# Optimization experiments

Measured on AMD Instinct MI355X. Metric: run time of the kernel, lower is better.

The kernel has to match this reference:

```python
import jax, jax.numpy as jnp
import numpy as np

NUM_ROI = 400
N_GRAPHS = 128
N_NODES = NUM_ROI * N_GRAPHS            # 51200
N_EDGES = N_NODES * 40                  # 2048000
EMB = [128, 128]
BN_EPS = 1e-5


def mish(x):
    return x * jnp.tanh(jax.nn.softplus(x))


def gcn_conv(x, row, col, ew, W, b, n_nodes):
    """PyG GCNConv: h = XW; add self-loops (w=1); sym-normalize; scatter-add; + bias."""
    h = x @ W                                            # [N, out]
    loops = jnp.arange(n_nodes, dtype=row.dtype)
    row_ = jnp.concatenate([row, loops])
    col_ = jnp.concatenate([col, loops])
    ew_ = jnp.concatenate([ew, jnp.ones((n_nodes,), ew.dtype)])
    deg = jax.ops.segment_sum(ew_, col_, num_segments=n_nodes)
    dinv = jnp.where(deg > 0, jax.lax.rsqrt(deg), 0.0)
    norm = dinv[row_] * ew_ * dinv[col_]                 # [E+N]
    msg = norm[:, None] * h[row_]                        # gather + scale
    out = jax.ops.segment_sum(msg, col_, num_segments=n_nodes)
    return out + b


def setup_inputs() -> dict:
    key = jax.random.key(0)
    ks = jax.random.split(key, 16)
    inp = {
        "x": jax.random.normal(ks[0], (N_NODES, NUM_ROI), jnp.float32),
        "edge_index": jax.random.randint(ks[1], (2, N_EDGES), 0, N_NODES, jnp.int64)
        if jax.config.jax_enable_x64 else jax.random.randint(ks[1], (2, N_EDGES), 0, N_NODES, jnp.int32),
        "edge_attr": jax.random.uniform(ks[2], (N_EDGES,), jnp.float32),
        "batch": jnp.repeat(jnp.arange(N_GRAPHS), NUM_ROI),
        "conv1_w": jax.random.normal(ks[3], (NUM_ROI, EMB[0]), jnp.float32) * 0.05,
        "conv1_b": jax.random.normal(ks[4], (EMB[0],), jnp.float32) * 0.05,
        "conv2_w": jax.random.normal(ks[5], (EMB[0], EMB[1]), jnp.float32) * 0.05,
        "conv2_b": jax.random.normal(ks[6], (EMB[1],), jnp.float32) * 0.05,
        "ro_w": jax.random.normal(ks[7], (EMB[1], 8), jnp.float32) * 0.05,
        "ro_b": jax.random.normal(ks[8], (8,), jnp.float32) * 0.05,
        "fc1_w": jax.random.normal(ks[9], (8 * NUM_ROI, NUM_ROI), jnp.float32) * 0.02,
        "fc1_b": jax.random.normal(ks[10], (NUM_ROI,), jnp.float32) * 0.02,
        "bn_gamma": jnp.ones((NUM_ROI,), jnp.float32),
        "bn_beta": jnp.zeros((NUM_ROI,), jnp.float32),
        "fc2_w": jax.random.normal(ks[11], (NUM_ROI, 2), jnp.float32) * 0.05,
        "fc2_b": jax.random.normal(ks[12], (2,), jnp.float32) * 0.05,
    }
    return inp


def reference(x, edge_index, edge_attr, batch,
              conv1_w, conv1_b, conv2_w, conv2_b,
              ro_w, ro_b, fc1_w, fc1_b, bn_gamma, bn_beta, fc2_w, fc2_b):
    n = x.shape[0]
    row, col = edge_index[0], edge_index[1]
    h = mish(gcn_conv(x, row, col, edge_attr, conv1_w, conv1_b, n))
    h = mish(gcn_conv(h, row, col, edge_attr, conv2_w, conv2_b, n))
    out = mish(h @ ro_w + ro_b)                          # [N, 8]
    feats = out.reshape(-1, NUM_ROI * 8)                 # [B, 3200]
    z = feats @ fc1_w + fc1_b                            # [B, 400]
    # BatchNorm1d (training mode: batch statistics, biased variance)
    mu = jnp.mean(z, axis=0)
    var = jnp.mean((z - mu) ** 2, axis=0)
    zn = (z - mu) * jax.lax.rsqrt(var + BN_EPS) * bn_gamma + bn_beta
    logits = mish(zn) @ fc2_w + fc2_b                    # [B, 2]
    return logits
```

## Files before the change

### kernel.cpp

```cpp
#include <hip/hip_runtime.h>
#include <hip/hip_fp16.h>
#include <math.h>

#define NN 51200
#define NE 2048000
#define F 128
#define NB 1000
#define EPB 2048
#define NBKT 200

typedef _Float16 half8 __attribute__((ext_vector_type(8)));
typedef float floatx4 __attribute__((ext_vector_type(4)));

__device__ __forceinline__ float mish_f(float x) {
  if (x > 20.0f) return x;
  float e = __expf(x);
  float w = 1.0f + e;
  w = w * w;
  return x * (w - 1.0f) / (w + 1.0f);
}

__global__ __launch_bounds__(256) void k_chist(const int* __restrict__ ei, unsigned* __restrict__ G) {
  __shared__ unsigned hist[NBKT];
  int blk = blockIdx.x, t = threadIdx.x;
  for (int i = t; i < NBKT; i += 256) hist[i] = 0u;
  __syncthreads();
  int base = blk * EPB;
  for (int it = 0; it < EPB; it += 256) {
    int dst = ei[NE + base + it + t];
    atomicAdd(&hist[dst >> 8], 1u);
  }
  __syncthreads();
  for (int i = t; i < NBKT; i += 256) G[(size_t)i * NB + blk] = hist[i];
}

__global__ __launch_bounds__(64) void k_bscan(unsigned* __restrict__ G, unsigned* __restrict__ btot) {
  int b = blockIdx.x, l = threadIdx.x;
  unsigned base = (unsigned)l * 16;
  unsigned loc[16];
  unsigned s = 0;
#pragma unroll
  for (int i = 0; i < 16; ++i) {
    unsigned idx = base + i;
    unsigned x = (idx < NB) ? G[(size_t)b * NB + idx] : 0u;
    loc[i] = s;
    s += x;
  }
  unsigned run = s;
#pragma unroll
  for (int off = 1; off < 64; off <<= 1) {
    unsigned y = __shfl_up(run, off);
    if (l >= off) run += y;
  }
  unsigned excl = run - s;
#pragma unroll
  for (int i = 0; i < 16; ++i) {
    unsigned idx = base + i;
    if (idx < NB) G[(size_t)b * NB + idx] = excl + loc[i];
  }
  if (l == 63) btot[b] = run;
}

__global__ __launch_bounds__(256) void k_bbase(const unsigned* __restrict__ btot, unsigned* __restrict__ bbase) {
  int t = threadIdx.x, lane = t & 63, wid = t >> 6;
  unsigned v = (t < NBKT) ? btot[t] : 0u;
  unsigned x = v;
#pragma unroll
  for (int off = 1; off < 64; off <<= 1) {
    unsigned y = __shfl_up(x, off);
    if (lane >= off) x += y;
  }
  __shared__ unsigned ws4[4];
  if (lane == 63) ws4[wid] = x;
  __syncthreads();
  unsigned woff = 0;
  for (int k = 0; k < wid; ++k) woff += ws4[k];
  if (t < NBKT) bbase[t] = woff + x - v;
  if (t == 255) bbase[NBKT] = woff + x;
}

__global__ __launch_bounds__(256) void k_cscat(const int* __restrict__ ei, const float* __restrict__ ew,
                                               const unsigned* __restrict__ G,
                                               const unsigned* __restrict__ bbase,
                                               uint2* __restrict__ E) {
  __shared__ unsigned cur[NBKT];
  int blk = blockIdx.x, t = threadIdx.x;
  for (int i = t; i < NBKT; i += 256) cur[i] = bbase[i] + G[(size_t)i * NB + blk];
  __syncthreads();
  int base = blk * EPB;
  for (int it = 0; it < EPB; it += 256) {
    int e = base + it + t;
    int dst = ei[NE + e];
    int src = ei[e];
    float w = ew[e];
    unsigned pos = atomicAdd(&cur[dst >> 8], 1u);
    E[pos] = make_uint2((unsigned)src | ((unsigned)(dst & 255) << 16), __float_as_uint(w));
  }
}

__global__ __launch_bounds__(256) void k_fcnt(const uint2* __restrict__ E, const unsigned* __restrict__ bbase,
                                              int* __restrict__ cnt, float* __restrict__ dinv) {
  __shared__ unsigned lc[256];
  __shared__ float ld[256];
  int b = blockIdx.x, t = threadIdx.x;
  lc[t] = 0u;
  ld[t] = 0.f;
  __syncthreads();
  unsigned e0 = bbase[b], e1 = bbase[b + 1];
  for (unsigned e = e0 + t; e < e1; e += 256) {
    uint2 v = E[e];
    unsigned node = (v.x >> 16) & 255u;
    atomicAdd(&lc[node], 1u);
    atomicAdd(&ld[node], __uint_as_float(v.y));
  }
  __syncthreads();
  cnt[b * 256 + t] = (int)lc[t];
  dinv[b * 256 + t] = rsqrtf(ld[t] + 1.0f);
}

__global__ __launch_bounds__(256) void k_scan1(const int* __restrict__ cnt, int* __restrict__ bsum) {
  int i = blockIdx.x * 256 + threadIdx.x;
  int s = cnt[i];
#pragma unroll
  for (int off = 1; off < 64; off <<= 1) s += __shfl_xor(s, off);
  __shared__ int wsum[4];
  if ((threadIdx.x & 63) == 0) wsum[threadIdx.x >> 6] = s;
  __syncthreads();
  if (threadIdx.x == 0) bsum[blockIdx.x] = wsum[0] + wsum[1] + wsum[2] + wsum[3];
}

__global__ __launch_bounds__(256) void k_scan2(const int* __restrict__ bsum, int* __restrict__ boff,
                                               int* __restrict__ rowptr) {
  int t = threadIdx.x;
  int lane = t & 63, wid = t >> 6;
  int v = (t < 200) ? bsum[t] : 0;
  int x = v;
#pragma unroll
  for (int off = 1; off < 64; off <<= 1) {
    int y = __shfl_up(x, off);
    if (lane >= off) x += y;
  }
  __shared__ int ws4[4];
  if (lane == 63) ws4[wid] = x;
  __syncthreads();
  int woff = 0;
  for (int k = 0; k < wid; ++k) woff += ws4[k];
  if (t < 200) boff[t] = woff + x - v;
  if (t == 255) rowptr[NN] = woff + x;
}

__global__ __launch_bounds__(256) void k_scan3(const int* __restrict__ cnt, const int* __restrict__ boff,
                                               int* __restrict__ rowptr) {
  int i = blockIdx.x * 256 + threadIdx.x;
  int t = threadIdx.x;
  int lane = t & 63, wid = t >> 6;
  int v = cnt[i];
  int x = v;
#pragma unroll
  for (int off = 1; off < 64; off <<= 1) {
    int y = __shfl_up(x, off);
    if (lane >= off) x += y;
  }
  __shared__ int ws4[4];
  if (lane == 63) ws4[wid] = x;
  __syncthreads();
  int woff = boff[blockIdx.x];
  for (int k = 0; k < wid; ++k) woff += ws4[k];
  rowptr[i] = woff + x - v;
}

__global__ __launch_bounds__(256) void k_fscat(const uint2* __restrict__ E, const unsigned* __restrict__ bbase,
                                               const int* __restrict__ rowptr, const float* __restrict__ dinv,
                                               int2* __restrict__ csr) {
  __shared__ int cur[256];
  int b = blockIdx.x, t = threadIdx.x;
  cur[t] = rowptr[b * 256 + t];
  __syncthreads();
  unsigned e0 = bbase[b], e1 = bbase[b + 1];
  for (unsigned e = e0 + t; e < e1; e += 256) {
    uint2 v = E[e];
    unsigned node = (v.x >> 16) & 255u;
    int src = (int)(v.x & 0xFFFFu);
    float w = dinv[src] * __uint_as_float(v.y);
    int p = atomicAdd(&cur[node], 1);
    csr[p] = make_int2(src, __float_as_int(w));
  }
}

__global__ void k_prep_w(const float* __restrict__ W, _Float16* __restrict__ Wt, int K) {
  int idx = blockIdx.x * blockDim.x + threadIdx.x;
  if (idx < K * 128) {
    int k = idx >> 7, n = idx & 127;
    Wt[n * K + k] = (_Float16)W[idx];
  }
}

template <bool A_IS_F32>
__global__ __launch_bounds__(256) void k_gemm16(const void* __restrict__ Av,
                                                const _Float16* __restrict__ Wt,
                                                __half* __restrict__ C, int K) {
  __shared__ _Float16 As[128][40];
  __shared__ _Float16 Bs[128][40];
  int t = threadIdx.x;
  int bm = blockIdx.x * 128;
  int w = t >> 6, l = t & 63, rr = l & 15, q = l >> 4;
  int si = t >> 1, sj = (t & 1) * 16;

  floatx4 acc[2][8];
#pragma unroll
  for (int a = 0; a < 2; ++a)
#pragma unroll
    for (int b = 0; b < 8; ++b) acc[a][b] = (floatx4){0.f, 0.f, 0.f, 0.f};

  for (int k0 = 0; k0 < K; k0 += 32) {
    if (A_IS_F32) {
      const float* A = (const float*)Av;
      half8 h0, h1;
      if (k0 + sj < K) {
        const float* ap = A + (size_t)(bm + si) * K + k0 + sj;
        float4 v0 = *(const float4*)(ap + 0);
        float4 v1 = *(const float4*)(ap + 4);
        float4 v2 = *(const float4*)(ap + 8);
        float4 v3 = *(const float4*)(ap + 12);
        h0 = (half8){(_Float16)v0.x, (_Float16)v0.y, (_Float16)v0.z, (_Float16)v0.w,
                     (_Float16)v1.x, (_Float16)v1.y, (_Float16)v1.z, (_Float16)v1.w};
        h1 = (half8){(_Float16)v2.x, (_Float16)v2.y, (_Float16)v2.z, (_Float16)v2.w,
                     (_Float16)v3.x, (_Float16)v3.y, (_Float16)v3.z, (_Float16)v3.w};
      } else {
        h0 = (half8){0, 0, 0, 0, 0, 0, 0, 0};
        h1 = h0;
      }
      *(half8*)&As[si][sj] = h0;
      *(half8*)&As[si][sj + 8] = h1;
    } else {
      const __half* A = (const __half*)Av;
      uint4 u0, u1;
      if (k0 + sj < K) {
        const __half* ap = A + (size_t)(bm + si) * K + k0 + sj;
        u0 = *(const uint4*)ap;
        u1 = *(const uint4*)(ap + 8);
      } else {
        u0 = make_uint4(0, 0, 0, 0);
        u1 = u0;
      }
      *(uint4*)&As[si][sj] = u0;
      *(uint4*)&As[si][sj + 8] = u1;
    }
    {
      uint4 u0, u1;
      if (k0 + sj < K) {
        const _Float16* wp = Wt + (size_t)si * K + k0 + sj;
        u0 = *(const uint4*)wp;
        u1 = *(const uint4*)(wp + 8);
      } else {
        u0 = make_uint4(0, 0, 0, 0);
        u1 = u0;
      }
      *(uint4*)&Bs[si][sj] = u0;
      *(uint4*)&Bs[si][sj + 8] = u1;
    }
    __syncthreads();

    half8 a0 = *(const half8*)&As[w * 32 + rr][q * 8];
    half8 a1 = *(const half8*)&As[w * 32 + 16 + rr][q * 8];
#pragma unroll
    for (int nt = 0; nt < 8; ++nt) {
      half8 b = *(const half8*)&Bs[nt * 16 + rr][q * 8];
      acc[0][nt] = __builtin_amdgcn_mfma_f32_16x16x32_f16(a0, b, acc[0][nt], 0, 0, 0);
      acc[1][nt] = __builtin_amdgcn_mfma_f32_16x16x32_f16(a1, b, acc[1][nt], 0, 0, 0);
    }
    __syncthreads();
  }
#pragma unroll
  for (int mt = 0; mt < 2; ++mt)
#pragma unroll
    for (int nt = 0; nt < 8; ++nt)
#pragma unroll
      for (int r4 = 0; r4 < 4; ++r4) {
        int row = bm + w * 32 + mt * 16 + q * 4 + r4;
        C[(size_t)row * 128 + nt * 16 + rr] = __float2half(acc[mt][nt][r4]);
      }
}

__global__ __launch_bounds__(256) void k_agg(const __half2* __restrict__ h, const int* __restrict__ rowptr,
                                             const int2* __restrict__ csr, const float* __restrict__ dinv,
                                             const float* __restrict__ bias, __half2* __restrict__ out) {
  unsigned lane = threadIdx.x & 63u;
  int n = blockIdx.x * 4 + (threadIdx.x >> 6);
  float di = dinv[n];
  float2 self = __half22float2(h[((unsigned)n << 6) + lane]);
  float sx = 0.f, sy = 0.f;
  int p = __builtin_amdgcn_readfirstlane(rowptr[n]);
  int p1 = __builtin_amdgcn_readfirstlane(rowptr[n + 1]);
  for (; p + 16 <= p1; p += 16) {
    int2 c[16];
#pragma unroll
    for (int u = 0; u < 16; ++u) c[u] = csr[p + u];
    float2 f[16];
#pragma unroll
    for (int u = 0; u < 16; ++u) f[u] = __half22float2(h[((unsigned)c[u].x << 6) + lane]);
#pragma unroll
    for (int u = 0; u < 16; ++u) {
      float w = __int_as_float(c[u].y);
      sx += w * f[u].x;
      sy += w * f[u].y;
    }
  }
  for (; p + 4 <= p1; p += 4) {
    int2 c[4];
#pragma unroll
    for (int u = 0; u < 4; ++u) c[u] = csr[p + u];
    float2 f[4];
#pragma unroll
    for (int u = 0; u < 4; ++u) f[u] = __half22float2(h[((unsigned)c[u].x << 6) + lane]);
#pragma unroll
    for (int u = 0; u < 4; ++u) {
      float w = __int_as_float(c[u].y);
      sx += w * f[u].x;
      sy += w * f[u].y;
    }
  }
  for (; p < p1; ++p) {
    int2 c0 = csr[p];
    float2 f0 = __half22float2(h[((unsigned)c0.x << 6) + lane]);
    float w = __int_as_float(c0.y);
    sx += w * f0.x;
    sy += w * f0.y;
  }
  float ax = di * (di * self.x + sx);
  float ay = di * (di * self.y + sy);
  float2 bb = ((const float2*)bias)[lane];
  out[((unsigned)n << 6) + lane] = __floats2half2_rn(mish_f(ax + bb.x), mish_f(ay + bb.y));
}

__global__ __launch_bounds__(256) void k_ro(const __half2* __restrict__ h, const float* __restrict__ rw,
                                            const float* __restrict__ rb, float* __restrict__ o8) {
  __shared__ float w[128 * 8];
  int t = threadIdx.x;
  for (int i = t; i < 1024; i += 256) w[i] = rw[i];
  __syncthreads();
  int n = blockIdx.x * 32 + (t >> 3);
  int k = t & 7;
  const __half2* hr = h + (size_t)n * 64;
  float acc = rb[k];
#pragma unroll 4
  for (int j = 0; j < 64; ++j) {
    float2 hv = __half22float2(hr[j]);
    acc += hv.x * w[(2 * j) * 8 + k] + hv.y * w[(2 * j + 1) * 8 + k];
  }
  o8[(size_t)n * 8 + k] = mish_f(acc);
}

__global__ void k_fc1_init(const float* __restrict__ b, float* __restrict__ z) {
  int i = blockIdx.x * blockDim.x + threadIdx.x;
  if (i < 128 * 400) z[i] = b[i % 400];
}

__global__ __launch_bounds__(448) void k_fc1(const float* __restrict__ feats, const float* __restrict__ w,
                                             float* __restrict__ z) {
  __shared__ float fs[8][128];
  int t = threadIdx.x;
  int kc = blockIdx.x * 128;
  int g0 = blockIdx.y * 8;
  for (int i = t; i < 1024; i += 448) {
    int g = i >> 7, k = i & 127;
    fs[g][k] = feats[(size_t)(g0 + g) * 3200 + kc + k];
  }
  __syncthreads();
  if (t < 400) {
    float a[8];
#pragma unroll
    for (int g = 0; g < 8; ++g) a[g] = 0.0f;
    for (int k = 0; k < 128; ++k) {
      float wv = w[(size_t)(kc + k) * 400 + t];
#pragma unroll
      for (int g = 0; g < 8; ++g) a[g] += fs[g][k] * wv;
    }
#pragma unroll
    for (int g = 0; g < 8; ++g) atomicAdd(&z[(size_t)(g0 + g) * 400 + t], a[g]);
  }
}

__global__ __launch_bounds__(128) void k_bn(const float* __restrict__ z, const float* __restrict__ gamma,
                                            const float* __restrict__ beta, float* __restrict__ gs,
                                            float* __restrict__ gb) {
  int j = blockIdx.x;
  int b = threadIdx.x;
  float v = z[b * 400 + j];
  float s = v, s2 = v * v;
#pragma unroll
  for (int off = 1; off < 64; off <<= 1) {
    s += __shfl_xor(s, off);
    s2 += __shfl_xor(s2, off);
  }
  __shared__ float ls[2], ls2[2];
  if ((b & 63) == 0) {
    ls[b >> 6] = s;
    ls2[b >> 6] = s2;
  }
  __syncthreads();
  if (b == 0) {
    float mu = (ls[0] + ls[1]) * (1.0f / 128.0f);
    float var = (ls2[0] + ls2[1]) * (1.0f / 128.0f) - mu * mu;
    float rs = rsqrtf(var + 1e-5f);
    float g = gamma[j] * rs;
    gs[j] = g;
    gb[j] = beta[j] - mu * g;
  }
}

__global__ __launch_bounds__(256) void k_fc2(const float* __restrict__ z, const float* __restrict__ gs,
                                             const float* __restrict__ gb, const float* __restrict__ w2,
                                             const float* __restrict__ b2, float* __restrict__ out) {
  int bg = blockIdx.x;
  int t = threadIdx.x;
  float a0 = 0.f, a1 = 0.f;
  for (int j = t; j < 400; j += 256) {
    float zn = z[bg * 400 + j] * gs[j] + gb[j];
    float m = mish_f(zn);
    a0 += m * w2[j * 2];
    a1 += m * w2[j * 2 + 1];
  }
#pragma unroll
  for (int off = 1; off < 64; off <<= 1) {
    a0 += __shfl_xor(a0, off);
    a1 += __shfl_xor(a1, off);
  }
  __shared__ float s0[4], s1[4];
  if ((t & 63) == 0) {
    s0[t >> 6] = a0;
    s1[t >> 6] = a1;
  }
  __syncthreads();
  if (t == 0) {
    out[bg * 2 + 0] = b2[0] + s0[0] + s0[1] + s0[2] + s0[3];
    out[bg * 2 + 1] = b2[1] + s1[0] + s1[1] + s1[2] + s1[3];
  }
}

extern "C" void kernel_launch(void* const* d_in, const int* in_sizes, int n_in,
                              void* d_out, int out_size, void* d_ws, size_t ws_size,
                              hipStream_t stream) {
  (void)in_sizes; (void)n_in; (void)out_size; (void)ws_size;
  const float* x   = (const float*)d_in[0];
  const int*   ei  = (const int*)d_in[1];
  const float* ew  = (const float*)d_in[2];
  const float* c1w = (const float*)d_in[4];
  const float* c1b = (const float*)d_in[5];
  const float* c2w = (const float*)d_in[6];
  const float* c2b = (const float*)d_in[7];
  const float* rw  = (const float*)d_in[8];
  const float* rb  = (const float*)d_in[9];
  const float* f1w = (const float*)d_in[10];
  const float* f1b = (const float*)d_in[11];
  const float* bng = (const float*)d_in[12];
  const float* bnb = (const float*)d_in[13];
  const float* f2w = (const float*)d_in[14];
  const float* f2b = (const float*)d_in[15];
  float* out = (float*)d_out;

  char* ws = (char*)d_ws;
  size_t off = 0;
  auto alloc = [&](size_t bytes) {
    void* p = ws + off;
    off = (off + bytes + 255) & ~(size_t)255;
    return p;
  };
  float* dinv    = (float*)alloc((size_t)NN * 4);
  int*   cnt     = (int*)alloc((size_t)NN * 4);
  int*   rowptr  = (int*)alloc((size_t)(NN + 1) * 4);
  int*   bsum    = (int*)alloc(200 * 4);
  int*   boff    = (int*)alloc(200 * 4);
  unsigned* G    = (unsigned*)alloc((size_t)NBKT * NB * 4);
  unsigned* btot = (unsigned*)alloc(NBKT * 4);
  unsigned* bbase= (unsigned*)alloc((NBKT + 1) * 4);
  int2*  csr     = (int2*)alloc((size_t)NE * 8);
  __half* A1     = (__half*)alloc((size_t)NN * F * 2);
  __half* B1     = (__half*)alloc((size_t)NN * F * 2);
  _Float16* Wt1  = (_Float16*)alloc((size_t)400 * 128 * 2);
  _Float16* Wt2  = (_Float16*)alloc((size_t)128 * 128 * 2);
  float* o8      = (float*)alloc((size_t)NN * 8 * 4);
  float* z       = (float*)alloc((size_t)128 * 400 * 4);
  float* gs      = (float*)alloc(400 * 4);
  float* gb      = (float*)alloc(400 * 4);

  uint2* E = (uint2*)A1;

  k_chist<<<NB, 256, 0, stream>>>(ei, G);
  k_bscan<<<NBKT, 64, 0, stream>>>(G, btot);
  k_bbase<<<1, 256, 0, stream>>>(btot, bbase);
  k_cscat<<<NB, 256, 0, stream>>>(ei, ew, G, bbase, E);
  k_fcnt<<<NBKT, 256, 0, stream>>>(E, bbase, cnt, dinv);
  k_scan1<<<NN / 256, 256, 0, stream>>>(cnt, bsum);
  k_scan2<<<1, 256, 0, stream>>>(bsum, boff, rowptr);
  k_scan3<<<NN / 256, 256, 0, stream>>>(cnt, boff, rowptr);
  k_fscat<<<NBKT, 256, 0, stream>>>(E, bbase, rowptr, dinv, csr);

  k_prep_w<<<(400 * 128 + 255) / 256, 256, 0, stream>>>(c1w, Wt1, 400);
  k_prep_w<<<(128 * 128 + 255) / 256, 256, 0, stream>>>(c2w, Wt2, 128);

  k_gemm16<true><<<NN / 128, 256, 0, stream>>>(x, Wt1, A1, 400);
  k_agg<<<NN / 4, 256, 0, stream>>>((const __half2*)A1, rowptr, csr, dinv, c1b, (__half2*)B1);
  k_gemm16<false><<<NN / 128, 256, 0, stream>>>(B1, Wt2, A1, 128);
  k_agg<<<NN / 4, 256, 0, stream>>>((const __half2*)A1, rowptr, csr, dinv, c2b, (__half2*)B1);
  k_ro<<<NN / 32, 256, 0, stream>>>((const __half2*)B1, rw, rb, o8);
  k_fc1_init<<<(128 * 400 + 255) / 256, 256, 0, stream>>>(f1b, z);
  {
    dim3 g(25, 16);
    k_fc1<<<g, 448, 0, stream>>>(o8, f1w, z);
  }
  k_bn<<<400, 128, 0, stream>>>(z, bng, bnb, gs, gb);
  k_fc2<<<128, 256, 0, stream>>>(z, gs, gb, f2w, f2b, out);
}
```

Baseline: 438.8 us.

## Split node features into four 32-column planes and pack CSR edges into 32 bits

Hidden features are stored as four column planes of 32 halves per node instead of one 128-wide row. The aggregation kernel gets one block group per plane, with each wavefront handling four edges at once via 16-lane groups, reduced by cross-lane shuffles. CSR entries now pack a 16-bit source index with an fp16 weight, halving edge-list traffic, and use nontemporal loads and stores. The aim is a smaller, L2-resident gather working set per pass and lighter edge reads, at the cost of reading the CSR four times, reduced edge-weight precision, and relying on node indices fitting in 16 bits, which holds here because the source is taken from a bucket-local encoding.

New measurement: 581.8 us. 1.33x slower.

```diff
diff --git a/kernel.cpp b/kernel.cpp
--- a/kernel.cpp
+++ b/kernel.cpp
@@ -8,6 +8,7 @@
 #define NB 1000
 #define EPB 2048
 #define NBKT 200
+#define QN (NN / 4)
 
 typedef _Float16 half8 __attribute__((ext_vector_type(8)));
 typedef float floatx4 __attribute__((ext_vector_type(4)));
@@ -171,7 +172,7 @@
 
 __global__ __launch_bounds__(256) void k_fscat(const uint2* __restrict__ E, const unsigned* __restrict__ bbase,
                                                const int* __restrict__ rowptr, const float* __restrict__ dinv,
-                                               int2* __restrict__ csr) {
+                                               unsigned* __restrict__ csr) {
   __shared__ int cur[256];
   int b = blockIdx.x, t = threadIdx.x;
   cur[t] = rowptr[b * 256 + t];
@@ -183,7 +184,8 @@
     int src = (int)(v.x & 0xFFFFu);
     float w = dinv[src] * __uint_as_float(v.y);
     int p = atomicAdd(&cur[node], 1);
-    csr[p] = make_int2(src, __float_as_int(w));
+    unsigned pk = (unsigned)src | ((unsigned)__half_as_ushort(__float2half_rn(w)) << 16);
+    __builtin_nontemporal_store(pk, &csr[p]);
   }
 }
 
@@ -234,15 +236,9 @@
       *(half8*)&As[si][sj + 8] = h1;
     } else {
       const __half* A = (const __half*)Av;
-      uint4 u0, u1;
-      if (k0 + sj < K) {
-        const __half* ap = A + (size_t)(bm + si) * K + k0 + sj;
-        u0 = *(const uint4*)ap;
-        u1 = *(const uint4*)(ap + 8);
-      } else {
-        u0 = make_uint4(0, 0, 0, 0);
-        u1 = u0;
-      }
+      const __half* ap = A + (size_t)(k0 >> 5) * ((size_t)NN * 32) + (size_t)(bm + si) * 32 + sj;
+      uint4 u0 = *(const uint4*)ap;
+      uint4 u1 = *(const uint4*)(ap + 8);
       *(uint4*)&As[si][sj] = u0;
       *(uint4*)&As[si][sj + 8] = u1;
     }
@@ -274,63 +270,73 @@
 #pragma unroll
   for (int mt = 0; mt < 2; ++mt)
 #pragma unroll
-    for (int nt = 0; nt < 8; ++nt)
+    for (int nt = 0; nt < 8; ++nt) {
+      int plane = nt >> 1;
+      int cw = (nt & 1) * 16 + rr;
 #pragma unroll
       for (int r4 = 0; r4 < 4; ++r4) {
         int row = bm + w * 32 + mt * 16 + q * 4 + r4;
-        C[(size_t)row * 128 + nt * 16 + rr] = __float2half(acc[mt][nt][r4]);
+        C[(size_t)plane * ((size_t)NN * 32) + (size_t)row * 32 + cw] = __float2half(acc[mt][nt][r4]);
       }
-}
-
-__global__ __launch_bounds__(256) void k_agg(const __half2* __restrict__ h, const int* __restrict__ rowptr,
-                                             const int2* __restrict__ csr, const float* __restrict__ dinv,
-                                             const float* __restrict__ bias, __half2* __restrict__ out) {
-  unsigned lane = threadIdx.x & 63u;
-  int n = blockIdx.x * 4 + (threadIdx.x >> 6);
+    }
+}
+
+__global__ __launch_bounds__(256) void k_aggq(const __half2* __restrict__ h,
+                                              const int* __restrict__ rowptr,
+                                              const unsigned* __restrict__ csr,
+                                              const float* __restrict__ dinv,
+                                              const float* __restrict__ bias,
+                                              __half2* __restrict__ out) {
+  int bid = blockIdx.x;
+  int qq = bid / QN;
+  int nb = bid - qq * QN;
+  unsigned t = threadIdx.x;
+  unsigned lane = t & 63u;
+  int n = nb * 4 + (int)(t >> 6);
+  unsigned g = lane >> 4;
+  unsigned fl = lane & 15u;
+  const __half2* hq = h + (size_t)qq * ((size_t)NN * 16);
   float di = dinv[n];
-  float2 self = __half22float2(h[((unsigned)n << 6) + lane]);
+  float2 self = __half22float2(hq[(unsigned)n * 16u + fl]);
+  float2 bb = ((const float2*)bias)[qq * 16 + fl];
+  int p0 = __builtin_amdgcn_readfirstlane(rowptr[n]);
+  int p1 = __builtin_amdgcn_readfirstlane(rowptr[n + 1]);
   float sx = 0.f, sy = 0.f;
-  int p = __builtin_amdgcn_readfirstlane(rowptr[n]);
-  int p1 = __builtin_amdgcn_readfirstlane(rowptr[n + 1]);
-  for (; p + 16 <= p1; p += 16) {
-    int2 c[16];
-#pragma unroll
-    for (int u = 0; u < 16; ++u) c[u] = csr[p + u];
-    float2 f[16];
-#pragma unroll
-    for (int u = 0; u < 16; ++u) f[u] = __half22float2(h[((unsigned)c[u].x << 6) + lane]);
-#pragma unroll
-    for (int u = 0; u < 16; ++u) {
-      float w = __int_as_float(c[u].y);
-      sx += w * f[u].x;
-      sy += w * f[u].y;
-    }
-  }
-  for (; p + 4 <= p1; p += 4) {
-    int2 c[4];
-#pragma unroll
-    for (int u = 0; u < 4; ++u) c[u] = csr[p + u];
+  int deg = p1 - p0;
+  int niter = (deg + 3) >> 2;
+  int last = p1 - 1;
+  for (int it = 0; it < niter; it += 4) {
+    unsigned c[4];
+#pragma unroll
+    for (int u = 0; u < 4; ++u) {
+      int ee = p0 + 4 * (it + u) + (int)g;
+      int ec = (ee <= last) ? ee : last;
+      unsigned cv = __builtin_nontemporal_load(&csr[ec]);
+      c[u] = (ee <= last) ? cv : (cv & 0xFFFFu);
+    }
     float2 f[4];
 #pragma unroll
-    for (int u = 0; u < 4; ++u) f[u] = __half22float2(h[((unsigned)c[u].x << 6) + lane]);
+    for (int u = 0; u < 4; ++u)
+      f[u] = __half22float2(hq[(c[u] & 0xFFFFu) * 16u + fl]);
 #pragma unroll
     for (int u = 0; u < 4; ++u) {
-      float w = __int_as_float(c[u].y);
-      sx += w * f[u].x;
-      sy += w * f[u].y;
-    }
-  }
-  for (; p < p1; ++p) {
-    int2 c0 = csr[p];
-    float2 f0 = __half22float2(h[((unsigned)c0.x << 6) + lane]);
-    float w = __int_as_float(c0.y);
-    sx += w * f0.x;
-    sy += w * f0.y;
-  }
+      float wv = __half2float(__ushort_as_half((unsigned short)(c[u] >> 16)));
+      sx += wv * f[u].x;
+      sy += wv * f[u].y;
+    }
+  }
+  sx += __shfl_xor(sx, 16);
+  sy += __shfl_xor(sy, 16);
+  sx += __shfl_xor(sx, 32);
+  sy += __shfl_xor(sy, 32);
   float ax = di * (di * self.x + sx);
   float ay = di * (di * self.y + sy);
-  float2 bb = ((const float2*)bias)[lane];
-  out[((unsigned)n << 6) + lane] = __floats2half2_rn(mish_f(ax + bb.x), mish_f(ay + bb.y));
+  if (g == 0) {
+    __half2 r = __floats2half2_rn(mish_f(ax + bb.x), mish_f(ay + bb.y));
+    unsigned rv = *reinterpret_cast<unsigned*>(&r);
+    __builtin_nontemporal_store(
+        rv, reinterpret_cast<unsigned*>(&out[(size_t)qq * ((size_t)NN * 16) + (unsigned)n * 16u + fl]));
+  }
 }
 
 __global__ __launch_bounds__(256) void k_ro(const __half2* __restrict__ h, const float* __restrict__ rw,
@@ -341,12 +347,16 @@
   __syncthreads();
   int n = blockIdx.x * 32 + (t >> 3);
   int k = t & 7;
-  const __half2* hr = h + (size_t)n * 64;
   float acc = rb[k];
+#pragma unroll
+  for (int p = 0; p < 4; ++p) {
+    const __half2* hr = h + (size_t)p * ((size_t)NN * 16) + (size_t)n * 16;
 #pragma unroll 4
-  for (int j = 0; j < 64; ++j) {
-    float2 hv = __half22float2(hr[j]);
-    acc += hv.x * w[(2 * j) * 8 + k] + hv.y * w[(2 * j + 1) * 8 + k];
+    for (int j = 0; j < 16; ++j) {
+      float2 hv = __half22float2(hr[j]);
+      int f0 = p * 32 + 2 * j;
+      acc += hv.x * w[f0 * 8 + k] + hv.y * w[(f0 + 1) * 8 + k];
+    }
   }
   o8[(size_t)n * 8 + k] = mish_f(acc);
 }
@@ -474,7 +484,7 @@
   unsigned* G    = (unsigned*)alloc((size_t)NBKT * NB * 4);
   unsigned* btot = (unsigned*)alloc(NBKT * 4);
   unsigned* bbase= (unsigned*)alloc((NBKT + 1) * 4);
-  int2*  csr     = (int2*)alloc((size_t)NE * 8);
+  unsigned* csr  = (unsigned*)alloc((size_t)NE * 4);
   __half* A1     = (__half*)alloc((size_t)NN * F * 2);
   __half* B1     = (__half*)alloc((size_t)NN * F * 2);
   _Float16* Wt1  = (_Float16*)alloc((size_t)400 * 128 * 2);
@@ -500,9 +510,9 @@
   k_prep_w<<<(128 * 128 + 255) / 256, 256, 0, stream>>>(c2w, Wt2, 128);
 
   k_gemm16<true><<<NN / 128, 256, 0, stream>>>(x, Wt1, A1, 400);
-  k_agg<<<NN / 4, 256, 0, stream>>>((const __half2*)A1, rowptr, csr, dinv, c1b, (__half2*)B1);
+  k_aggq<<<4 * QN, 256, 0, stream>>>((const __half2*)A1, rowptr, csr, dinv, c1b, (__half2*)B1);
   k_gemm16<false><<<NN / 128, 256, 0, stream>>>(B1, Wt2, A1, 128);
-  k_agg<<<NN / 4, 256, 0, stream>>>((const __half2*)A1, rowptr, csr, dinv, c2b, (__half2*)B1);
+  k_aggq<<<4 * QN, 256, 0, stream>>>((const __half2*)A1, rowptr, csr, dinv, c2b, (__half2*)B1);
   k_ro<<<NN / 32, 256, 0, stream>>>((const __half2*)B1, rw, rb, o8);
   k_fc1_init<<<(128 * 400 + 255) / 256, 256, 0, stream>>>(f1b, z);
   {
```

## Split CSR by source quarter and co-schedule aggregation across nodes for L2 locality

Applied to the files above, without the earlier changes.

Each node's edge list is now partitioned by source-id quarter, and each wave aggregates 13 consecutive nodes one source quarter at a time. At any moment the gathered feature rows therefore come from a narrower window, which is meant to improve cache hit rates. CSR entries shrink from 8 to 4 bytes by packing a 16-bit source id with an fp16 weight, and they use nontemporal loads and stores. The cost is larger count and scan arrays, extra register pressure from 13 accumulators per lane, and reduced edge-weight precision.

Result: slower. 574.2 us (+30.8%).

```diff
diff --git a/kernel.cpp b/kernel.cpp
--- a/kernel.cpp
+++ b/kernel.cpp
@@ -8,6 +8,9 @@
 #define NB 1000
 #define EPB 2048
 #define NBKT 200
+#define QDIV 12800
+#define CO_BLOCKS 1024
+#define NPW 13
 
 typedef _Float16 half8 __attribute__((ext_vector_type(8)));
 typedef float floatx4 __attribute__((ext_vector_type(4)));
@@ -99,22 +102,24 @@
 }
 
 __global__ __launch_bounds__(256) void k_fcnt(const uint2* __restrict__ E, const unsigned* __restrict__ bbase,
-                                              int* __restrict__ cnt, float* __restrict__ dinv) {
-  __shared__ unsigned lc[256];
+                                              int* __restrict__ cnt4, float* __restrict__ dinv) {
+  __shared__ unsigned lc[1024];
   __shared__ float ld[256];
   int b = blockIdx.x, t = threadIdx.x;
-  lc[t] = 0u;
+  for (int i = t; i < 1024; i += 256) lc[i] = 0u;
   ld[t] = 0.f;
   __syncthreads();
   unsigned e0 = bbase[b], e1 = bbase[b + 1];
   for (unsigned e = e0 + t; e < e1; e += 256) {
     uint2 v = E[e];
     unsigned node = (v.x >> 16) & 255u;
-    atomicAdd(&lc[node], 1u);
+    unsigned src = v.x & 0xFFFFu;
+    unsigned q = src / QDIV;
+    atomicAdd(&lc[(node << 2) | q], 1u);
     atomicAdd(&ld[node], __uint_as_float(v.y));
   }
   __syncthreads();
-  cnt[b * 256 + t] = (int)lc[t];
+  for (int i = t; i < 1024; i += 256) cnt4[(size_t)b * 1024 + i] = (int)lc[i];
   dinv[b * 256 + t] = rsqrtf(ld[t] + 1.0f);
 }
 
@@ -130,11 +135,19 @@
 }
 
 __global__ __launch_bounds__(256) void k_scan2(const int* __restrict__ bsum, int* __restrict__ boff,
-                                               int* __restrict__ rowptr) {
+                                               int* __restrict__ rowptr4) {
   int t = threadIdx.x;
   int lane = t & 63, wid = t >> 6;
-  int v = (t < 200) ? bsum[t] : 0;
-  int x = v;
+  int loc[4];
+  int s = 0;
+#pragma unroll
+  for (int i = 0; i < 4; ++i) {
+    int idx = t * 4 + i;
+    int v = (idx < 800) ? bsum[idx] : 0;
+    loc[i] = s;
+    s += v;
+  }
+  int x = s;
 #pragma unroll
   for (int off = 1; off < 64; off <<= 1) {
     int y = __shfl_up(x, off);
@@ -145,8 +158,13 @@
   __syncthreads();
   int woff = 0;
   for (int k = 0; k < wid; ++k) woff += ws4[k];
-  if (t < 200) boff[t] = woff + x - v;
-  if (t == 255) rowptr[NN] = woff + x;
+  int base = woff + x - s;
+#pragma unroll
+  for (int i = 0; i < 4; ++i) {
+    int idx = t * 4 + i;
+    if (idx < 800) boff[idx] = base + loc[i];
+  }
+  if (t == 255) rowptr4[4 * NN] = woff + x;
 }
 
 __global__ __launch_bounds__(256) void k_scan3(const int* __restrict__ cnt, const int* __restrict__ boff,
@@ -170,20 +188,22 @@
 }
 
 __global__ __launch_bounds__(256) void k_fscat(const uint2* __restrict__ E, const unsigned* __restrict__ bbase,
-                                               const int* __restrict__ rowptr, const float* __restrict__ dinv,
-                                               int2* __restrict__ csr) {
-  __shared__ int cur[256];
+                                               const int* __restrict__ rowptr4, const float* __restrict__ dinv,
+                                               unsigned* __restrict__ csr) {
+  __shared__ int cur[1024];
   int b = blockIdx.x, t = threadIdx.x;
-  cur[t] = rowptr[b * 256 + t];
+  for (int i = t; i < 1024; i += 256) cur[i] = rowptr4[(size_t)b * 1024 + i];
   __syncthreads();
   unsigned e0 = bbase[b], e1 = bbase[b + 1];
   for (unsigned e = e0 + t; e < e1; e += 256) {
     uint2 v = E[e];
     unsigned node = (v.x >> 16) & 255u;
-    int src = (int)(v.x & 0xFFFFu);
+    unsigned src = v.x & 0xFFFFu;
+    unsigned q = src / QDIV;
     float w = dinv[src] * __uint_as_float(v.y);
-    int p = atomicAdd(&cur[node], 1);
-    csr[p] = make_int2(src, __float_as_int(w));
+    int p = atomicAdd(&cur[(node << 2) | q], 1);
+    unsigned pk = src | ((unsigned)__half_as_ushort(__float2half_rn(w)) << 16);
+    __builtin_nontemporal_store(pk, &csr[p]);
   }
 }
 
@@ -282,55 +302,85 @@
       }
 }
 
-__global__ __launch_bounds__(256) void k_agg(const __half2* __restrict__ h, const int* __restrict__ rowptr,
-                                             const int2* __restrict__ csr, const float* __restrict__ dinv,
-                                             const float* __restrict__ bias, __half2* __restrict__ out) {
-  unsigned lane = threadIdx.x & 63u;
-  int n = blockIdx.x * 4 + (threadIdx.x >> 6);
-  float di = dinv[n];
-  float2 self = __half22float2(h[((unsigned)n << 6) + lane]);
-  float sx = 0.f, sy = 0.f;
-  int p = __builtin_amdgcn_readfirstlane(rowptr[n]);
-  int p1 = __builtin_amdgcn_readfirstlane(rowptr[n + 1]);
-  for (; p + 16 <= p1; p += 16) {
-    int2 c[16];
-#pragma unroll
-    for (int u = 0; u < 16; ++u) c[u] = csr[p + u];
-    float2 f[16];
-#pragma unroll
-    for (int u = 0; u < 16; ++u) f[u] = __half22float2(h[((unsigned)c[u].x << 6) + lane]);
-#pragma unroll
-    for (int u = 0; u < 16; ++u) {
-      float w = __int_as_float(c[u].y);
-      sx += w * f[u].x;
-      sy += w * f[u].y;
+__global__ __launch_bounds__(256) void k_aggco(const __half2* __restrict__ h,
+                                               const int* __restrict__ rowptr4,
+                                               const unsigned* __restrict__ csr,
+                                               const float* __restrict__ dinv,
+                                               const float* __restrict__ bias,
+                                               __half2* __restrict__ out) {
+  unsigned t = threadIdx.x;
+  unsigned lane = t & 63u;
+  int wv = blockIdx.x * 4 + (int)(t >> 6);
+  int n0 = wv * NPW;
+  float sx[NPW], sy[NPW];
+#pragma unroll
+  for (int j = 0; j < NPW; ++j) {
+    sx[j] = 0.f;
+    sy[j] = 0.f;
+  }
+  for (int q = 0; q < 4; ++q) {
+#pragma unroll
+    for (int j = 0; j < NPW; ++j) {
+      int n = n0 + j;
+      if (n < NN) {
+        int p = __builtin_amdgcn_readfirstlane(rowptr4[n * 4 + q]);
+        int p1 = __builtin_amdgcn_readfirstlane(rowptr4[n * 4 + q + 1]);
+        float ax = sx[j], ay = sy[j];
+        for (; p + 8 <= p1; p += 8) {
+          unsigned c[8];
+#pragma unroll
+          for (int u = 0; u < 8; ++u) c[u] = __builtin_nontemporal_load(&csr[p + u]);
+          float2 f[8];
+#pragma unroll
+          for (int u = 0; u < 8; ++u)
+            f[u] = __half22float2(h[((c[u] & 0xFFFFu) << 6) + lane]);
+#pragma unroll
+          for (int u = 0; u < 8; ++u) {
+            float w = __half2float(__ushort_as_half((unsigned short)(c[u] >> 16)));
+            ax += w * f[u].x;
+            ay += w * f[u].y;
+          }
+        }
+        if (p < p1) {
+          int last = p1 - 1;
+          for (; p < p1; p += 4) {
+            unsigned c[4];
+#pragma unroll
+            for (int u = 0; u < 4; ++u) {
+              int ee = p + u;
+              int ec = (ee <= last) ? ee : last;
+              unsigned cv = __builtin_nontemporal_load(&csr[ec]);
+              c[u] = (ee <= last) ? cv : (cv & 0xFFFFu);
+            }
+            float2 f[4];
+#pragma unroll
+            for (int u = 0; u < 4; ++u)
+              f[u] = __half22float2(h[((c[u] & 0xFFFFu) << 6) + lane]);
+#pragma unroll
+            for (int u = 0; u < 4; ++u) {
+              float w = __half2float(__ushort_as_half((unsigned short)(c[u] >> 16)));
+              ax += w * f[u].x;
+              ay += w * f[u].y;
+            }
+          }
+        }
+        sx[j] = ax;
+        sy[j] = ay;
+      }
     }
   }
-  for (; p + 4 <= p1; p += 4) {
-    int2 c[4];
-#pragma unroll
-    for (int u = 0; u < 4; ++u) c[u] = csr[p + u];
-    float2 f[4];
-#pragma unroll
-    for (int u = 0; u < 4; ++u) f[u] = __half22float2(h[((unsigned)c[u].x << 6) + lane]);
-#pragma unroll
-    for (int u = 0; u < 4; ++u) {
-      float w = __int_as_float(c[u].y);
-      sx += w * f[u].x;
-      sy += w * f[u].y;
+  float2 bb = ((const float2*)bias)[lane];
+#pragma unroll
+  for (int j = 0; j < NPW; ++j) {
+    int n = n0 + j;
+    if (n < NN) {
+      float di = dinv[n];
+      float2 self = __half22float2(h[((unsigned)n << 6) + lane]);
+      float ax = di * (di * self.x + sx[j]);
+      float ay = di * (di * self.y + sy[j]);
+      out[((unsigned)n << 6) + lane] = __floats2half2_rn(mish_f(ax + bb.x), mish_f(ay + bb.y));
     }
   }
-  for (; p < p1; ++p) {
-    int2 c0 = csr[p];
-    float2 f0 = __half22float2(h[((unsigned)c0.x << 6) + lane]);
-    float w = __int_as_float(c0.y);
-    sx += w * f0.x;
-    sy += w * f0.y;
-  }
-  float ax = di * (di * self.x + sx);
-  float ay = di * (di * self.y + sy);
-  float2 bb = ((const float2*)bias)[lane];
-  out[((unsigned)n << 6) + lane] = __floats2half2_rn(mish_f(ax + bb.x), mish_f(ay + bb.y));
 }
 
 __global__ __launch_bounds__(256) void k_ro(const __half2* __restrict__ h, const float* __restrict__ rw,
@@ -467,14 +517,14 @@
     return p;
   };
   float* dinv    = (float*)alloc((size_t)NN * 4);
-  int*   cnt     = (int*)alloc((size_t)NN * 4);
-  int*   rowptr  = (int*)alloc((size_t)(NN + 1) * 4);
-  int*   bsum    = (int*)alloc(200 * 4);
-  int*   boff    = (int*)alloc(200 * 4);
+  int*   cnt4    = (int*)alloc((size_t)4 * NN * 4);
+  int*   rowptr4 = (int*)alloc((size_t)(4 * NN + 1) * 4);
+  int*   bsum    = (int*)alloc(800 * 4);
+  int*   boff    = (int*)alloc(800 * 4);
   unsigned* G    = (unsigned*)alloc((size_t)NBKT * NB * 4);
   unsigned* btot = (unsigned*)alloc(NBKT * 4);
   unsigned* bbase= (unsigned*)alloc((NBKT + 1) * 4);
-  int2*  csr     = (int2*)alloc((size_t)NE * 8);
+  unsigned* csr  = (unsigned*)alloc((size_t)NE * 4 + 64);
   __half* A1     = (__half*)alloc((size_t)NN * F * 2);
   __half* B1     = (__half*)alloc((size_t)NN * F * 2);
   _Float16* Wt1  = (_Float16*)alloc((size_t)400 * 128 * 2);
@@ -490,19 +540,19 @@
   k_bscan<<<NBKT, 64, 0, stream>>>(G, btot);
   k_bbase<<<1, 256, 0, stream>>>(btot, bbase);
   k_cscat<<<NB, 256, 0, stream>>>(ei, ew, G, bbase, E);
-  k_fcnt<<<NBKT, 256, 0, stream>>>(E, bbase, cnt, dinv);
-  k_scan1<<<NN / 256, 256, 0, stream>>>(cnt, bsum);
-  k_scan2<<<1, 256, 0, stream>>>(bsum, boff, rowptr);
-  k_scan3<<<NN / 256, 256, 0, stream>>>(cnt, boff, rowptr);
-  k_fscat<<<NBKT, 256, 0, stream>>>(E, bbase, rowptr, dinv, csr);
+  k_fcnt<<<NBKT, 256, 0, stream>>>(E, bbase, cnt4, dinv);
+  k_scan1<<<4 * NN / 256, 256, 0, stream>>>(cnt4, bsum);
+  k_scan2<<<1, 256, 0, stream>>>(bsum, boff, rowptr4);
+  k_scan3<<<4 * NN / 256, 256, 0, stream>>>(cnt4, boff, rowptr4);
+  k_fscat<<<NBKT, 256, 0, stream>>>(E, bbase, rowptr4, dinv, csr);
 
   k_prep_w<<<(400 * 128 + 255) / 256, 256, 0, stream>>>(c1w, Wt1, 400);
   k_prep_w<<<(128 * 128 + 255) / 256, 256, 0, stream>>>(c2w, Wt2, 128);
 
   k_gemm16<true><<<NN / 128, 256, 0, stream>>>(x, Wt1, A1, 400);
-  k_agg<<<NN / 4, 256, 0, stream>>>((const __half2*)A1, rowptr, csr, dinv, c1b, (__half2*)B1);
+  k_aggco<<<CO_BLOCKS, 256, 0, stream>>>((const __half2*)A1, rowptr4, csr, dinv, c1b, (__half2*)B1);
   k_gemm16<false><<<NN / 128, 256, 0, stream>>>(B1, Wt2, A1, 128);
-  k_agg<<<NN / 4, 256, 0, stream>>>((const __half2*)A1, rowptr, csr, dinv, c2b, (__half2*)B1);
+  k_aggco<<<CO_BLOCKS, 256, 0, stream>>>((const __half2*)A1, rowptr4, csr, dinv, c2b, (__half2*)B1);
   k_ro<<<NN / 32, 256, 0, stream>>>((const __half2*)B1, rw, rb, o8);
   k_fc1_init<<<(128 * 400 + 255) / 256, 256, 0, stream>>>(f1b, z);
   {
```

## Build CSR with global atomics and pack edges as 16-bit index plus fp16 weight

Applied to the files above, without the earlier changes.

Replaces the two-level bucket-sort CSR construction (histogram, scans, bucket scatter, per-bucket count and final scatter) with a direct global-atomic degree count, a prefix scan, and a global-atomic scatter. CSR entries shrink from 8 to 4 bytes by packing the 16-bit source index with an fp16 normalized weight, which cuts the memory traffic of both aggregation passes. The weight-transpose and zero-init kernels are merged into one launch. The fc1 bias initialization is dropped, since training-mode BatchNorm subtracts the batch mean and cancels it. The risks are heavier contention on global atomics and reduced edge-weight precision.

New measurement: 637.0 us. 1.45x slower.

```diff
diff --git a/kernel.cpp b/kernel.cpp
--- a/kernel.cpp
+++ b/kernel.cpp
@@ -5,9 +5,6 @@
 #define NN 51200
 #define NE 2048000
 #define F 128
-#define NB 1000
-#define EPB 2048
-#define NBKT 200
 
 typedef _Float16 half8 __attribute__((ext_vector_type(8)));
 typedef float floatx4 __attribute__((ext_vector_type(4)));
@@ -20,102 +17,27 @@
   return x * (w - 1.0f) / (w + 1.0f);
 }
 
-__global__ __launch_bounds__(256) void k_chist(const int* __restrict__ ei, unsigned* __restrict__ G) {
-  __shared__ unsigned hist[NBKT];
-  int blk = blockIdx.x, t = threadIdx.x;
-  for (int i = t; i < NBKT; i += 256) hist[i] = 0u;
-  __syncthreads();
-  int base = blk * EPB;
-  for (int it = 0; it < EPB; it += 256) {
-    int dst = ei[NE + base + it + t];
-    atomicAdd(&hist[dst >> 8], 1u);
-  }
-  __syncthreads();
-  for (int i = t; i < NBKT; i += 256) G[(size_t)i * NB + blk] = hist[i];
-}
-
-__global__ __launch_bounds__(64) void k_bscan(unsigned* __restrict__ G, unsigned* __restrict__ btot) {
-  int b = blockIdx.x, l = threadIdx.x;
-  unsigned base = (unsigned)l * 16;
-  unsigned loc[16];
-  unsigned s = 0;
-#pragma unroll
-  for (int i = 0; i < 16; ++i) {
-    unsigned idx = base + i;
-    unsigned x = (idx < NB) ? G[(size_t)b * NB + idx] : 0u;
-    loc[i] = s;
-    s += x;
-  }
-  unsigned run = s;
-#pragma unroll
-  for (int off = 1; off < 64; off <<= 1) {
-    unsigned y = __shfl_up(run, off);
-    if (l >= off) run += y;
-  }
-  unsigned excl = run - s;
-#pragma unroll
-  for (int i = 0; i < 16; ++i) {
-    unsigned idx = base + i;
-    if (idx < NB) G[(size_t)b * NB + idx] = excl + loc[i];
-  }
-  if (l == 63) btot[b] = run;
-}
-
-__global__ __launch_bounds__(256) void k_bbase(const unsigned* __restrict__ btot, unsigned* __restrict__ bbase) {
-  int t = threadIdx.x, lane = t & 63, wid = t >> 6;
-  unsigned v = (t < NBKT) ? btot[t] : 0u;
-  unsigned x = v;
-#pragma unroll
-  for (int off = 1; off < 64; off <<= 1) {
-    unsigned y = __shfl_up(x, off);
-    if (lane >= off) x += y;
-  }
-  __shared__ unsigned ws4[4];
-  if (lane == 63) ws4[wid] = x;
-  __syncthreads();
-  unsigned woff = 0;
-  for (int k = 0; k < wid; ++k) woff += ws4[k];
-  if (t < NBKT) bbase[t] = woff + x - v;
-  if (t == 255) bbase[NBKT] = woff + x;
-}
-
-__global__ __launch_bounds__(256) void k_cscat(const int* __restrict__ ei, const float* __restrict__ ew,
-                                               const unsigned* __restrict__ G,
-                                               const unsigned* __restrict__ bbase,
-                                               uint2* __restrict__ E) {
-  __shared__ unsigned cur[NBKT];
-  int blk = blockIdx.x, t = threadIdx.x;
-  for (int i = t; i < NBKT; i += 256) cur[i] = bbase[i] + G[(size_t)i * NB + blk];
-  __syncthreads();
-  int base = blk * EPB;
-  for (int it = 0; it < EPB; it += 256) {
-    int e = base + it + t;
-    int dst = ei[NE + e];
-    int src = ei[e];
-    float w = ew[e];
-    unsigned pos = atomicAdd(&cur[dst >> 8], 1u);
-    E[pos] = make_uint2((unsigned)src | ((unsigned)(dst & 255) << 16), __float_as_uint(w));
-  }
-}
-
-__global__ __launch_bounds__(256) void k_fcnt(const uint2* __restrict__ E, const unsigned* __restrict__ bbase,
-                                              int* __restrict__ cnt, float* __restrict__ dinv) {
-  __shared__ unsigned lc[256];
-  __shared__ float ld[256];
-  int b = blockIdx.x, t = threadIdx.x;
-  lc[t] = 0u;
-  ld[t] = 0.f;
-  __syncthreads();
-  unsigned e0 = bbase[b], e1 = bbase[b + 1];
-  for (unsigned e = e0 + t; e < e1; e += 256) {
-    uint2 v = E[e];
-    unsigned node = (v.x >> 16) & 255u;
-    atomicAdd(&lc[node], 1u);
-    atomicAdd(&ld[node], __uint_as_float(v.y));
-  }
-  __syncthreads();
-  cnt[b * 256 + t] = (int)lc[t];
-  dinv[b * 256 + t] = rsqrtf(ld[t] + 1.0f);
+__global__ __launch_bounds__(256) void k_init(const float* __restrict__ W1, const float* __restrict__ W2,
+                                              _Float16* __restrict__ Wt1, _Float16* __restrict__ Wt2,
+                                              float* __restrict__ zbase) {
+  int idx = blockIdx.x * 256 + threadIdx.x;
+  if (idx < 51200) {
+    int k = idx >> 7, n = idx & 127;
+    Wt1[n * 400 + k] = (_Float16)W1[idx];
+  } else {
+    int i2 = idx - 51200;
+    int k = i2 >> 7, n = i2 & 127;
+    Wt2[n * 128 + k] = (_Float16)W2[i2];
+  }
+  for (int i = idx; i < 3 * NN; i += 67584) zbase[i] = 0.0f;
+}
+
+__global__ __launch_bounds__(256) void k_cnt(const int* __restrict__ ei, const float* __restrict__ ew,
+                                             int* __restrict__ cnt, float* __restrict__ degf) {
+  int e = blockIdx.x * 256 + threadIdx.x;
+  int dst = ei[NE + e];
+  atomicAdd(&cnt[dst], 1);
+  atomicAdd(&degf[dst], ew[e]);
 }
 
 __global__ __launch_bounds__(256) void k_scan1(const int* __restrict__ cnt, int* __restrict__ bsum) {
@@ -150,7 +72,8 @@
 }
 
 __global__ __launch_bounds__(256) void k_scan3(const int* __restrict__ cnt, const int* __restrict__ boff,
-                                               int* __restrict__ rowptr) {
+                                               const float* __restrict__ degf, int* __restrict__ rowptr,
+                                               int* __restrict__ cur, float* __restrict__ dinv) {
   int i = blockIdx.x * 256 + threadIdx.x;
   int t = threadIdx.x;
   int lane = t & 63, wid = t >> 6;
@@ -166,33 +89,22 @@
   __syncthreads();
   int woff = boff[blockIdx.x];
   for (int k = 0; k < wid; ++k) woff += ws4[k];
-  rowptr[i] = woff + x - v;
-}
-
-__global__ __launch_bounds__(256) void k_fscat(const uint2* __restrict__ E, const unsigned* __restrict__ bbase,
-                                               const int* __restrict__ rowptr, const float* __restrict__ dinv,
-                                               int2* __restrict__ csr) {
-  __shared__ int cur[256];
-  int b = blockIdx.x, t = threadIdx.x;
-  cur[t] = rowptr[b * 256 + t];
-  __syncthreads();
-  unsigned e0 = bbase[b], e1 = bbase[b + 1];
-  for (unsigned e = e0 + t; e < e1; e += 256) {
-    uint2 v = E[e];
-    unsigned node = (v.x >> 16) & 255u;
-    int src = (int)(v.x & 0xFFFFu);
-    float w = dinv[src] * __uint_as_float(v.y);
-    int p = atomicAdd(&cur[node], 1);
-    csr[p] = make_int2(src, __float_as_int(w));
-  }
-}
-
-__global__ void k_prep_w(const float* __restrict__ W, _Float16* __restrict__ Wt, int K) {
-  int idx = blockIdx.x * blockDim.x + threadIdx.x;
-  if (idx < K * 128) {
-    int k = idx >> 7, n = idx & 127;
-    Wt[n * K + k] = (_Float16)W[idx];
-  }
+  int rp = woff + x - v;
+  rowptr[i] = rp;
+  cur[i] = rp;
+  dinv[i] = rsqrtf(degf[i] + 1.0f);
+}
+
+__global__ __launch_bounds__(256) void k_scat(const int* __restrict__ ei, const float* __restrict__ ew,
+                                              const float* __restrict__ dinv, int* __restrict__ cur,
+                                              unsigned* __restrict__ csr) {
+  int e = blockIdx.x * 256 + threadIdx.x;
+  int dst = ei[NE + e];
+  int src = ei[e];
+  float w = dinv[src] * ew[e];
+  int p = atomicAdd(&cur[dst], 1);
+  unsigned pk = (unsigned)src | ((unsigned)__half_as_ushort(__float2half_rn(w)) << 16);
+  __builtin_nontemporal_store(pk, &csr[p]);
 }
 
 template <bool A_IS_F32>
@@ -283,7 +195,7 @@
 }
 
 __global__ __launch_bounds__(256) void k_agg(const __half2* __restrict__ h, const int* __restrict__ rowptr,
-                                             const int2* __restrict__ csr, const float* __restrict__ dinv,
+                                             const unsigned* __restrict__ csr, const float* __restrict__ dinv,
                                              const float* __restrict__ bias, __half2* __restrict__ out) {
   unsigned lane = threadIdx.x & 63u;
   int n = blockIdx.x * 4 + (threadIdx.x >> 6);
@@ -293,37 +205,37 @@
   int p = __builtin_amdgcn_readfirstlane(rowptr[n]);
   int p1 = __builtin_amdgcn_readfirstlane(rowptr[n + 1]);
   for (; p + 16 <= p1; p += 16) {
-    int2 c[16];
+    unsigned c[16];
 #pragma unroll
     for (int u = 0; u < 16; ++u) c[u] = csr[p + u];
     float2 f[16];
 #pragma unroll
-    for (int u = 0; u < 16; ++u) f[u] = __half22float2(h[((unsigned)c[u].x << 6) + lane]);
+    for (int u = 0; u < 16; ++u) f[u] = __half22float2(h[((c[u] & 0xFFFFu) << 6) + lane]);
 #pragma unroll
     for (int u = 0; u < 16; ++u) {
-      float w = __int_as_float(c[u].y);
+      float w = __half2float(__ushort_as_half((unsigned short)(c[u] >> 16)));
       sx += w * f[u].x;
       sy += w * f[u].y;
     }
   }
   for (; p + 4 <= p1; p += 4) {
-    int2 c[4];
+    unsigned c[4];
 #pragma unroll
     for (int u = 0; u < 4; ++u) c[u] = csr[p + u];
     float2 f[4];
 #pragma unroll
-    for (int u = 0; u < 4; ++u) f[u] = __half22float2(h[((unsigned)c[u].x << 6) + lane]);
+    for (int u = 0; u < 4; ++u) f[u] = __half22float2(h[((c[u] & 0xFFFFu) << 6) + lane]);
 #pragma unroll
     for (int u = 0; u < 4; ++u) {
-      float w = __int_as_float(c[u].y);
+      float w = __half2float(__ushort_as_half((unsigned short)(c[u] >> 16)));
       sx += w * f[u].x;
       sy += w * f[u].y;
     }
   }
   for (; p < p1; ++p) {
-    int2 c0 = csr[p];
-    float2 f0 = __half22float2(h[((unsigned)c0.x << 6) + lane]);
-    float w = __int_as_float(c0.y);
+    unsigned c0 = csr[p];
+    float2 f0 = __half22float2(h[((c0 & 0xFFFFu) << 6) + lane]);
+    float w = __half2float(__ushort_as_half((unsigned short)(c0 >> 16)));
     sx += w * f0.x;
     sy += w * f0.y;
   }
@@ -349,11 +261,6 @@
     acc += hv.x * w[(2 * j) * 8 + k] + hv.y * w[(2 * j + 1) * 8 + k];
   }
   o8[(size_t)n * 8 + k] = mish_f(acc);
-}
-
-__global__ void k_fc1_init(const float* __restrict__ b, float* __restrict__ z) {
-  int i = blockIdx.x * blockDim.x + threadIdx.x;
-  if (i < 128 * 400) z[i] = b[i % 400];
 }
 
 __global__ __launch_bounds__(448) void k_fc1(const float* __restrict__ feats, const float* __restrict__ w,
@@ -452,7 +359,6 @@
   const float* rw  = (const float*)d_in[8];
   const float* rb  = (const float*)d_in[9];
   const float* f1w = (const float*)d_in[10];
-  const float* f1b = (const float*)d_in[11];
   const float* bng = (const float*)d_in[12];
   const float* bnb = (const float*)d_in[13];
   const float* f2w = (const float*)d_in[14];
@@ -466,45 +372,35 @@
     off = (off + bytes + 255) & ~(size_t)255;
     return p;
   };
+  int*   cnt     = (int*)alloc((size_t)NN * 4);
+  float* degf    = (float*)alloc((size_t)NN * 4);
+  float* z       = (float*)alloc((size_t)NN * 4);
   float* dinv    = (float*)alloc((size_t)NN * 4);
-  int*   cnt     = (int*)alloc((size_t)NN * 4);
   int*   rowptr  = (int*)alloc((size_t)(NN + 1) * 4);
+  int*   cur     = (int*)alloc((size_t)NN * 4);
   int*   bsum    = (int*)alloc(200 * 4);
   int*   boff    = (int*)alloc(200 * 4);
-  unsigned* G    = (unsigned*)alloc((size_t)NBKT * NB * 4);
-  unsigned* btot = (unsigned*)alloc(NBKT * 4);
-  unsigned* bbase= (unsigned*)alloc((NBKT + 1) * 4);
-  int2*  csr     = (int2*)alloc((size_t)NE * 8);
+  unsigned* csr  = (unsigned*)alloc((size_t)NE * 4 + 64);
   __half* A1     = (__half*)alloc((size_t)NN * F * 2);
   __half* B1     = (__half*)alloc((size_t)NN * F * 2);
   _Float16* Wt1  = (_Float16*)alloc((size_t)400 * 128 * 2);
   _Float16* Wt2  = (_Float16*)alloc((size_t)128 * 128 * 2);
   float* o8      = (float*)alloc((size_t)NN * 8 * 4);
-  float* z       = (float*)alloc((size_t)128 * 400 * 4);
   float* gs      = (float*)alloc(400 * 4);
   float* gb      = (float*)alloc(400 * 4);
 
-  uint2* E = (uint2*)A1;
-
-  k_chist<<<NB, 256, 0, stream>>>(ei, G);
-  k_bscan<<<NBKT, 64, 0, stream>>>(G, btot);
-  k_bbase<<<1, 256, 0, stream>>>(btot, bbase);
-  k_cscat<<<NB, 256, 0, stream>>>(ei, ew, G, bbase, E);
-  k_fcnt<<<NBKT, 256, 0, stream>>>(E, bbase, cnt, dinv);
+  k_init<<<264, 256, 0, stream>>>(c1w, c2w, Wt1, Wt2, (float*)cnt);
+  k_cnt<<<NE / 256, 256, 0, stream>>>(ei, ew, cnt, degf);
   k_scan1<<<NN / 256, 256, 0, stream>>>(cnt, bsum);
   k_scan2<<<1, 256, 0, stream>>>(bsum, boff, rowptr);
-  k_scan3<<<NN / 256, 256, 0, stream>>>(cnt, boff, rowptr);
-  k_fscat<<<NBKT, 256, 0, stream>>>(E, bbase, rowptr, dinv, csr);
-
-  k_prep_w<<<(400 * 128 + 255) / 256, 256, 0, stream>>>(c1w, Wt1, 400);
-  k_prep_w<<<(128 * 128 + 255) / 256, 256, 0, stream>>>(c2w, Wt2, 128);
+  k_scan3<<<NN / 256, 256, 0, stream>>>(cnt, boff, degf, rowptr, cur, dinv);
+  k_scat<<<NE / 256, 256, 0, stream>>>(ei, ew, dinv, cur, csr);
 
   k_gemm16<true><<<NN / 128, 256, 0, stream>>>(x, Wt1, A1, 400);
   k_agg<<<NN / 4, 256, 0, stream>>>((const __half2*)A1, rowptr, csr, dinv, c1b, (__half2*)B1);
   k_gemm16<false><<<NN / 128, 256, 0, stream>>>(B1, Wt2, A1, 128);
   k_agg<<<NN / 4, 256, 0, stream>>>((const __half2*)A1, rowptr, csr, dinv, c2b, (__half2*)B1);
   k_ro<<<NN / 32, 256, 0, stream>>>((const __half2*)B1, rw, rb, o8);
-  k_fc1_init<<<(128 * 400 + 255) / 256, 256, 0, stream>>>(f1b, z);
   {
     dim3 g(25, 16);
     k_fc1<<<g, 448, 0, stream>>>(o8, f1w, z);
```
